# Kernel tuning notes

Hardware: AMD Instinct MI355X
Metric: run time of the kernel (lower is better)

The kernel has to match this reference:

```python
import jax, jax.numpy as jnp
import numpy as np

HEADS = 16
DIM_HEAD = 64
SCALE = DIM_HEAD ** -0.5


def setup_inputs() -> dict:
    key = jax.random.key(0)
    ks = jax.random.split(key, 7)
    b, n, m, d = 2, 2048, 2048, 1024
    inner = HEADS * DIM_HEAD  # 1024
    patch_embed = jax.random.normal(ks[0], (b, n, d), dtype=jnp.float32)
    pixel_embed = jax.random.normal(ks[1], (b, m, d), dtype=jnp.float32)
    s = 1.0 / np.sqrt(d)
    Wq = jax.random.normal(ks[2], (d, inner), dtype=jnp.float32) * s
    Wk = jax.random.normal(ks[3], (d, inner), dtype=jnp.float32) * s
    Wv = jax.random.normal(ks[4], (d, inner), dtype=jnp.float32) * s
    Wo = jax.random.normal(ks[5], (inner, d), dtype=jnp.float32) * (1.0 / np.sqrt(inner))
    bo = jax.random.normal(ks[6], (d,), dtype=jnp.float32) * 0.01
    return {"patch_embed": patch_embed, "pixel_embed": pixel_embed,
            "Wq": Wq, "Wk": Wk, "Wv": Wv, "Wo": Wo, "bo": bo}


def reference(patch_embed, pixel_embed, Wq, Wk, Wv, Wo, bo):
    b, n, _ = patch_embed.shape
    h, dh = HEADS, DIM_HEAD
    # projections
    q = patch_embed @ Wq  # [b, n, h*dh]
    k = pixel_embed @ Wk  # [b, m, h*dh]
    v = pixel_embed @ Wv  # [b, m, h*dh]
    # split heads: [b, seq, h, dh]
    q = q.reshape(b, n, h, dh)
    k = k.reshape(b, -1, h, dh)
    v = v.reshape(b, -1, h, dh)
    sim = jnp.einsum('bihd,bjhd->bhij', q, k) * SCALE  # [b, h, n, m]
    attn = jax.nn.softmax(sim, axis=-1)
    out = jnp.einsum('bhij,bjhd->bihd', attn, v)  # [b, n, h, dh]
    out = out.reshape(b, n, h * dh)
    return out @ Wo + bo  # [b, n, query_dim]
```

## Files before the change

kernel.cpp:

```cpp
#include <hip/hip_runtime.h>

#define SEQ 2048
#define DMODEL 1024
#define HEADS 16
#define DH 64
#define QSCALE 0.180336880f

typedef __attribute__((ext_vector_type(8))) short short8;
typedef __attribute__((ext_vector_type(4))) float f32x4;
typedef __attribute__((ext_vector_type(16))) float f32x16;
typedef __attribute__((ext_vector_type(2))) unsigned int uint2v;
typedef __attribute__((ext_vector_type(4))) unsigned int uint4v;

__device__ __forceinline__ ushort f2bf(float x) {
  union { float f; unsigned u; } v; v.f = x;
  return (ushort)((v.u + 0x7fffu + ((v.u >> 16) & 1u)) >> 16);
}

__device__ __forceinline__ void gld16(const ushort* g, ushort* l) {
  __builtin_amdgcn_global_load_lds(
      (const __attribute__((address_space(1))) unsigned int*)g,
      (__attribute__((address_space(3))) unsigned int*)l, 16, 0, 0);
}

__global__ __launch_bounds__(256) void prologue(
    const float* __restrict__ patch, const float* __restrict__ pixel,
    const float* __restrict__ W0, const float* __restrict__ W1,
    const float* __restrict__ W2, const float* __restrict__ W3,
    ushort* __restrict__ pb, ushort* __restrict__ xb,
    ushort* __restrict__ O0, ushort* __restrict__ O1,
    ushort* __restrict__ O2, ushort* __restrict__ O3) {
  const int z = blockIdx.z;
  const int tx = threadIdx.x, ty = threadIdx.y;
  if (z < 2) {
    const float4* in = (const float4*)(z ? pixel : patch);
    ushort4* out = (ushort4*)(z ? xb : pb);
    const int base = (blockIdx.y * 32 + blockIdx.x) * 256 + ty * 32 + tx;
#pragma unroll
    for (int rep = 0; rep < 4; ++rep) {
      const int i = base + rep * 262144;
      float4 f = in[i];
      out[i] = make_ushort4(f2bf(f.x), f2bf(f.y), f2bf(f.z), f2bf(f.w));
    }
    return;
  }
  __shared__ float tile[32][33];
  const int zz = z - 2;
  const float* in = zz == 0 ? W0 : zz == 1 ? W1 : zz == 2 ? W2 : W3;
  ushort* out = zz == 0 ? O0 : zz == 1 ? O1 : zz == 2 ? O2 : O3;
  const float scale = zz == 0 ? QSCALE : 1.0f;
  const int n0 = blockIdx.x * 32, k0 = blockIdx.y * 32;
#pragma unroll
  for (int i = 0; i < 4; ++i)
    tile[ty + i * 8][tx] = in[(size_t)(k0 + ty + i * 8) * DMODEL + n0 + tx];
  __syncthreads();
#pragma unroll
  for (int i = 0; i < 4; ++i)
    out[(size_t)(n0 + ty + i * 8) * DMODEL + k0 + tx] =
        f2bf(tile[tx][ty + i * 8] * scale);
}

__global__ __launch_bounds__(256) void mfma_gemm_qkv(
    const ushort* __restrict__ pb, const ushort* __restrict__ xb,
    const ushort* __restrict__ wqt, const ushort* __restrict__ wkt,
    const ushort* __restrict__ wvt, ushort* __restrict__ qws,
    ushort* __restrict__ kws, ushort* __restrict__ vws) {
  __shared__ __align__(16) ushort As[128 * 64];
  __shared__ __align__(16) ushort Bs[128 * 64];
  const int z = blockIdx.z;
  const ushort* A = (z == 0) ? pb : xb;
  const ushort* Bt = (z == 0) ? wqt : (z == 1) ? wkt : wvt;

  const int t = threadIdx.x;
  const int w = t >> 6, lane = t & 63, ln = lane & 15, q = lane >> 4;
  const int wm = w & 1, wn = w >> 1;
  const int row0 = blockIdx.y * 128, col0 = blockIdx.x * 128;
  const int sw = ln & 7;

  f32x4 acc[4][4];
#pragma unroll
  for (int i = 0; i < 4; ++i)
#pragma unroll
    for (int j = 0; j < 4; ++j) acc[i][j] = (f32x4){0.f, 0.f, 0.f, 0.f};

  for (int k0 = 0; k0 < DMODEL; k0 += 64) {
    __syncthreads();
#pragma unroll
    for (int rep = 0; rep < 4; ++rep) {
      const int u0 = rep * 256 + w * 64;
      const int u = u0 + lane;
      const int r = u >> 3, gl = (u & 7) ^ (r & 7);
      gld16(&A[(size_t)(row0 + r) * DMODEL + k0 + gl * 8], &As[u0 * 8]);
      gld16(&Bt[(size_t)(col0 + r) * DMODEL + k0 + gl * 8], &Bs[u0 * 8]);
    }
    __syncthreads();
#pragma unroll
    for (int ks = 0; ks < 2; ++ks) {
      short8 af[4], bf[4];
#pragma unroll
      for (int rt = 0; rt < 4; ++rt)
        af[rt] = *(const short8*)&As[(wm * 64 + rt * 16 + ln) * 64 +
                                     (((ks * 4 + q) ^ sw) * 8)];
#pragma unroll
      for (int ct = 0; ct < 4; ++ct)
        bf[ct] = *(const short8*)&Bs[(wn * 64 + ct * 16 + ln) * 64 +
                                     (((ks * 4 + q) ^ sw) * 8)];
#pragma unroll
      for (int rt = 0; rt < 4; ++rt)
#pragma unroll
        for (int ct = 0; ct < 4; ++ct)
          acc[rt][ct] = __builtin_amdgcn_mfma_f32_16x16x32_bf16(af[rt], bf[ct],
                                                                acc[rt][ct], 0, 0, 0);
    }
  }

  if (z < 2) {
    ushort* dst = z == 0 ? qws : kws;
#pragma unroll
    for (int rt = 0; rt < 4; ++rt)
#pragma unroll
      for (int ct = 0; ct < 4; ++ct) {
        const int c = col0 + wn * 64 + ct * 16 + ln;
#pragma unroll
        for (int reg = 0; reg < 4; ++reg) {
          const int r = row0 + wm * 64 + rt * 16 + q * 4 + reg;
          dst[(size_t)r * DMODEL + c] = f2bf(acc[rt][ct][reg]);
        }
      }
  } else {
#pragma unroll
    for (int rt = 0; rt < 4; ++rt)
#pragma unroll
      for (int ct = 0; ct < 4; ++ct) {
        const int c = col0 + wn * 64 + ct * 16 + ln;
        const int hh = c >> 6, d = c & 63;
        const int r0 = row0 + wm * 64 + rt * 16 + q * 4;
        const int bb = r0 >> 11, s0 = r0 & (SEQ - 1);
        ushort4 u4 = make_ushort4(f2bf(acc[rt][ct][0]), f2bf(acc[rt][ct][1]),
                                  f2bf(acc[rt][ct][2]), f2bf(acc[rt][ct][3]));
        *(ushort4*)&vws[((size_t)(bb * HEADS + hh) * DH + d) * SEQ + s0] = u4;
      }
  }
}

__global__ __launch_bounds__(256, 2) void flash_mfma(
    const ushort* __restrict__ Qg, const ushort* __restrict__ Kg,
    const ushort* __restrict__ Vg, ushort* __restrict__ Og) {
  __shared__ __align__(16) ushort Kst[2][64 * 64];
  __shared__ __align__(16) ushort Vst[2][64 * 64];

  const int t = threadIdx.x;
  const int w = t >> 6, lane = t & 63;
  const int l31 = lane & 31, hi = lane >> 5, l7 = lane & 7, l8 = lane >> 3;
  const int bh = blockIdx.x;
  const int qt = blockIdx.y;
  const int b = bh >> 4, h = bh & 15;

  const ushort* qrow = Qg + ((size_t)b * SEQ) * DMODEL + h * DH;
  const ushort* krow = Kg + ((size_t)b * SEQ) * DMODEL + h * DH;
  const ushort* vg = Vg + (size_t)bh * DH * SEQ;

  short8 qf[4];
#pragma unroll
  for (int ks = 0; ks < 4; ++ks)
    qf[ks] = *(const short8*)
        &qrow[(size_t)(qt * 128 + w * 32 + l31) * DMODEL + ks * 16 + hi * 8];

  f32x16 acc_o[2];
#pragma unroll
  for (int db = 0; db < 2; ++db)
#pragma unroll
    for (int e = 0; e < 16; ++e) acc_o[db][e] = 0.f;
  float l_i = 0.f;

  const int fbase = (w & 1) * 4;
  const bool isV = (w >= 2);
  const int swz = (l7 ^ l8) * 8;

  {
#pragma unroll
    for (int i = 0; i < 4; ++i) {
      const int f = fbase + i;
      if (!isV)
        gld16(&krow[(size_t)(f * 8 + l8) * DMODEL + swz], &Kst[0][f * 512]);
      else
        gld16(&vg[(size_t)(f * 8 + l8) * SEQ + swz], &Vst[0][f * 512]);
    }
  }
  __syncthreads();

  for (int kt = 0; kt < SEQ / 64; ++kt) {
    const int cur = kt & 1;
    if (kt + 1 < SEQ / 64) {
#pragma unroll
      for (int i = 0; i < 4; ++i) {
        const int f = fbase + i;
        if (!isV)
          gld16(&krow[(size_t)((kt + 1) * 64 + f * 8 + l8) * DMODEL + swz],
                &Kst[cur ^ 1][f * 512]);
        else
          gld16(&vg[(size_t)(f * 8 + l8) * SEQ + (kt + 1) * 64 + swz],
                &Vst[cur ^ 1][f * 512]);
      }
    }

    const ushort* Kc = &Kst[cur][0];
    const ushort* Vc = &Vst[cur][0];

    f32x16 accs[2];
#pragma unroll
    for (int kb = 0; kb < 2; ++kb)
#pragma unroll
      for (int e = 0; e < 16; ++e) accs[kb][e] = 0.f;
#pragma unroll
    for (int kb = 0; kb < 2; ++kb)
#pragma unroll
      for (int ks = 0; ks < 4; ++ks) {
        const short8 kf = *(const short8*)
            &Kc[(kb * 32 + l31) * 64 + (((ks * 2 + hi) ^ l7) * 8)];
        accs[kb] = __builtin_amdgcn_mfma_f32_32x32x16_bf16(kf, qf[ks],
                                                           accs[kb], 0, 0, 0);
      }

    short8 vf[4][2];
#pragma unroll
    for (int sg = 0; sg < 4; ++sg)
#pragma unroll
      for (int db = 0; db < 2; ++db)
        vf[sg][db] = *(const short8*)
            &Vc[(db * 32 + l31) * 64 + (((sg * 2 + hi) ^ l7) * 8)];

#pragma unroll
    for (int kb = 0; kb < 2; ++kb)
#pragma unroll
      for (int e = 0; e < 16; ++e) {
        const float p = __builtin_amdgcn_exp2f(accs[kb][e]);
        accs[kb][e] = p;
        l_i += p;
      }

    short8 pa[4];
#pragma unroll
    for (int kb = 0; kb < 2; ++kb) {
      unsigned wq[4][2];
#pragma unroll
      for (int o = 0; o < 4; ++o) {
        asm("v_cvt_pk_bf16_f32 %0, %1, %2"
            : "=v"(wq[o][0])
            : "v"(accs[kb][4 * o + 0]), "v"(accs[kb][4 * o + 1]));
        asm("v_cvt_pk_bf16_f32 %0, %1, %2"
            : "=v"(wq[o][1])
            : "v"(accs[kb][4 * o + 2]), "v"(accs[kb][4 * o + 3]));
      }
#pragma unroll
      for (int sl = 0; sl < 2; ++sl) {
        uint2v r02 = __builtin_amdgcn_permlane32_swap(wq[2 * sl][0],
                                                      wq[2 * sl + 1][0],
                                                      false, false);
        uint2v r13 = __builtin_amdgcn_permlane32_swap(wq[2 * sl][1],
                                                      wq[2 * sl + 1][1],
                                                      false, false);
        uint4v pk = {r02.x, r13.x, r02.y, r13.y};
        pa[kb * 2 + sl] = __builtin_bit_cast(short8, pk);
      }
    }

#pragma unroll
    for (int sg = 0; sg < 4; ++sg)
#pragma unroll
      for (int db = 0; db < 2; ++db)
        acc_o[db] = __builtin_amdgcn_mfma_f32_32x32x16_bf16(pa[sg], vf[sg][db],
                                                            acc_o[db], 0, 0, 0);

    __syncthreads();
  }

  l_i += __shfl_xor(l_i, 32);
  const float inv = 1.0f / l_i;
#pragma unroll
  for (int o = 0; o < 4; ++o)
#pragma unroll
    for (int r0 = 0; r0 < 4; ++r0) {
      const int row = o * 8 + r0 + 4 * hi;
      const float invr = __shfl(inv, row, 64);
      const int s = qt * 128 + w * 32 + row;
#pragma unroll
      for (int db = 0; db < 2; ++db)
        Og[(size_t)(b * SEQ + s) * DMODEL + h * DH + db * 32 + l31] =
            f2bf(acc_o[db][4 * o + r0] * invr);
    }
}

__global__ __launch_bounds__(256) void mfma_gemm_out(const ushort* __restrict__ A,
                                                     const ushort* __restrict__ Bt,
                                                     const float* __restrict__ bias,
                                                     float* __restrict__ dst) {
  __shared__ __align__(16) ushort As[64 * 64];
  __shared__ __align__(16) ushort Bs[128 * 64];
  const int t = threadIdx.x;
  const int w = t >> 6, lane = t & 63, ln = lane & 15, q = lane >> 4;
  const int wm = w & 1, wn = w >> 1;
  const int row0 = blockIdx.y * 64, col0 = blockIdx.x * 128;
  const int sw = ln & 7;

  f32x4 acc[2][4];
#pragma unroll
  for (int i = 0; i < 2; ++i)
#pragma unroll
    for (int j = 0; j < 4; ++j) acc[i][j] = (f32x4){0.f, 0.f, 0.f, 0.f};

  for (int k0 = 0; k0 < DMODEL; k0 += 64) {
    __syncthreads();
#pragma unroll
    for (int rep = 0; rep < 2; ++rep) {
      const int u0 = rep * 256 + w * 64;
      const int u = u0 + lane;
      const int r = u >> 3, gl = (u & 7) ^ (r & 7);
      gld16(&A[(size_t)(row0 + r) * DMODEL + k0 + gl * 8], &As[u0 * 8]);
    }
#pragma unroll
    for (int rep = 0; rep < 4; ++rep) {
      const int u0 = rep * 256 + w * 64;
      const int u = u0 + lane;
      const int r = u >> 3, gl = (u & 7) ^ (r & 7);
      gld16(&Bt[(size_t)(col0 + r) * DMODEL + k0 + gl * 8], &Bs[u0 * 8]);
    }
    __syncthreads();
#pragma unroll
    for (int ks = 0; ks < 2; ++ks) {
      short8 af[2], bf[4];
#pragma unroll
      for (int rt = 0; rt < 2; ++rt)
        af[rt] = *(const short8*)&As[(wm * 32 + rt * 16 + ln) * 64 +
                                     (((ks * 4 + q) ^ sw) * 8)];
#pragma unroll
      for (int ct = 0; ct < 4; ++ct)
        bf[ct] = *(const short8*)&Bs[(wn * 64 + ct * 16 + ln) * 64 +
                                     (((ks * 4 + q) ^ sw) * 8)];
#pragma unroll
      for (int rt = 0; rt < 2; ++rt)
#pragma unroll
        for (int ct = 0; ct < 4; ++ct)
          acc[rt][ct] = __builtin_amdgcn_mfma_f32_16x16x32_bf16(af[rt], bf[ct],
                                                                acc[rt][ct], 0, 0, 0);
    }
  }

#pragma unroll
  for (int rt = 0; rt < 2; ++rt)
#pragma unroll
    for (int ct = 0; ct < 4; ++ct) {
      const int c = col0 + wn * 64 + ct * 16 + ln;
      const float bi = bias[c];
#pragma unroll
      for (int reg = 0; reg < 4; ++reg) {
        const int r = row0 + wm * 32 + rt * 16 + q * 4 + reg;
        dst[(size_t)r * DMODEL + c] = acc[rt][ct][reg] + bi;
      }
    }
}

extern "C" void kernel_launch(void* const* d_in, const int* in_sizes, int n_in,
                              void* d_out, int out_size, void* d_ws,
                              size_t ws_size, hipStream_t stream) {
  const float* patch = (const float*)d_in[0];
  const float* pixel = (const float*)d_in[1];
  const float* Wq = (const float*)d_in[2];
  const float* Wk = (const float*)d_in[3];
  const float* Wv = (const float*)d_in[4];
  const float* Wo = (const float*)d_in[5];
  const float* bo = (const float*)d_in[6];
  float* out = (float*)d_out;

  const size_t E = (size_t)2 * SEQ * DMODEL;
  const size_t W = (size_t)DMODEL * DMODEL;
  ushort* pb  = (ushort*)d_ws;
  ushort* xb  = pb + E;
  ushort* wqt = xb + E;
  ushort* wkt = wqt + W;
  ushort* wvt = wkt + W;
  ushort* wot = wvt + W;
  ushort* qws = wot + W;
  ushort* kws = qws + E;
  ushort* vws = kws + E;
  ushort* aws = vws + E;

  prologue<<<dim3(32, 32, 6), dim3(32, 8), 0, stream>>>(
      patch, pixel, Wq, Wk, Wv, Wo, pb, xb, wqt, wkt, wvt, wot);
  mfma_gemm_qkv<<<dim3(8, 32, 3), 256, 0, stream>>>(pb, xb, wqt, wkt, wvt,
                                                    qws, kws, vws);
  flash_mfma<<<dim3(32, 16), 256, 0, stream>>>(qws, kws, vws, aws);
  mfma_gemm_out<<<dim3(8, 64), 256, 0, stream>>>(aws, wot, bo, out);
}
```

Before: 190.8 us.

## Deepen flash attention K/V staging to four-buffer pipeline with vmcnt waits

Replaces the double-buffered K/V shared-memory staging with a four-slot ring that prefetches three tiles ahead. The loop is unrolled by four, and the full __syncthreads is replaced with explicit s_waitcnt vmcnt plus s_barrier so only the oldest tile's loads must land before compute. The change also adds s_setprio around the MFMA blocks and starts the first QK MFMA from a zero vector instead of zeroing accumulators. Shared memory doubles to 64KB per block, which may limit the two-blocks-per-CU occupancy target.

```diff
diff --git a/kernel.cpp b/kernel.cpp
--- a/kernel.cpp
+++ b/kernel.cpp
@@ -146,8 +146,8 @@
 __global__ __launch_bounds__(256, 2) void flash_mfma(
     const ushort* __restrict__ Qg, const ushort* __restrict__ Kg,
     const ushort* __restrict__ Vg, ushort* __restrict__ Og) {
-  __shared__ __align__(16) ushort Kst[2][64 * 64];
-  __shared__ __align__(16) ushort Vst[2][64 * 64];
+  __shared__ __align__(16) ushort Kst[4][64 * 64];
+  __shared__ __align__(16) ushort Vst[4][64 * 64];
 
   const int t = threadIdx.x;
   const int w = t >> 6, lane = t & 63;
@@ -173,107 +173,113 @@
     for (int e = 0; e < 16; ++e) acc_o[db][e] = 0.f;
   float l_i = 0.f;
 
+  f32x16 ZERO;
+#pragma unroll
+  for (int e = 0; e < 16; ++e) ZERO[e] = 0.f;
+
   const int fbase = (w & 1) * 4;
   const bool isV = (w >= 2);
   const int swz = (l7 ^ l8) * 8;
 
-  {
-#pragma unroll
-    for (int i = 0; i < 4; ++i) {
-      const int f = fbase + i;
-      if (!isV)
-        gld16(&krow[(size_t)(f * 8 + l8) * DMODEL + swz], &Kst[0][f * 512]);
-      else
-        gld16(&vg[(size_t)(f * 8 + l8) * SEQ + swz], &Vst[0][f * 512]);
-    }
-  }
-  __syncthreads();
-
-  for (int kt = 0; kt < SEQ / 64; ++kt) {
-    const int cur = kt & 1;
-    if (kt + 1 < SEQ / 64) {
+  auto stage = [&](int tile, ushort* Kb, ushort* Vb) {
+    if (!isV) {
 #pragma unroll
       for (int i = 0; i < 4; ++i) {
         const int f = fbase + i;
-        if (!isV)
-          gld16(&krow[(size_t)((kt + 1) * 64 + f * 8 + l8) * DMODEL + swz],
-                &Kst[cur ^ 1][f * 512]);
-        else
-          gld16(&vg[(size_t)(f * 8 + l8) * SEQ + (kt + 1) * 64 + swz],
-                &Vst[cur ^ 1][f * 512]);
+        gld16(&krow[(size_t)(tile * 64 + f * 8 + l8) * DMODEL + swz],
+              &Kb[f * 512]);
       }
-    }
-
-    const ushort* Kc = &Kst[cur][0];
-    const ushort* Vc = &Vst[cur][0];
-
-    f32x16 accs[2];
-#pragma unroll
-    for (int kb = 0; kb < 2; ++kb)
-#pragma unroll
-      for (int e = 0; e < 16; ++e) accs[kb][e] = 0.f;
-#pragma unroll
-    for (int kb = 0; kb < 2; ++kb)
-#pragma unroll
-      for (int ks = 0; ks < 4; ++ks) {
-        const short8 kf = *(const short8*)
-            &Kc[(kb * 32 + l31) * 64 + (((ks * 2 + hi) ^ l7) * 8)];
-        accs[kb] = __builtin_amdgcn_mfma_f32_32x32x16_bf16(kf, qf[ks],
-                                                           accs[kb], 0, 0, 0);
+    } else {
+#pragma unroll
+      for (int i = 0; i < 4; ++i) {
+        const int f = fbase + i;
+        gld16(&vg[(size_t)(f * 8 + l8) * SEQ + tile * 64 + swz],
+              &Vb[f * 512]);
       }
-
-    short8 vf[4][2];
-#pragma unroll
-    for (int sg = 0; sg < 4; ++sg)
-#pragma unroll
-      for (int db = 0; db < 2; ++db)
-        vf[sg][db] = *(const short8*)
-            &Vc[(db * 32 + l31) * 64 + (((sg * 2 + hi) ^ l7) * 8)];
-
-#pragma unroll
-    for (int kb = 0; kb < 2; ++kb)
-#pragma unroll
-      for (int e = 0; e < 16; ++e) {
-        const float p = __builtin_amdgcn_exp2f(accs[kb][e]);
-        accs[kb][e] = p;
-        l_i += p;
-      }
-
-    short8 pa[4];
-#pragma unroll
-    for (int kb = 0; kb < 2; ++kb) {
-      unsigned wq[4][2];
-#pragma unroll
-      for (int o = 0; o < 4; ++o) {
-        asm("v_cvt_pk_bf16_f32 %0, %1, %2"
-            : "=v"(wq[o][0])
-            : "v"(accs[kb][4 * o + 0]), "v"(accs[kb][4 * o + 1]));
-        asm("v_cvt_pk_bf16_f32 %0, %1, %2"
-            : "=v"(wq[o][1])
-            : "v"(accs[kb][4 * o + 2]), "v"(accs[kb][4 * o + 3]));
-      }
-#pragma unroll
-      for (int sl = 0; sl < 2; ++sl) {
-        uint2v r02 = __builtin_amdgcn_permlane32_swap(wq[2 * sl][0],
-                                                      wq[2 * sl + 1][0],
-                                                      false, false);
-        uint2v r13 = __builtin_amdgcn_permlane32_swap(wq[2 * sl][1],
-                                                      wq[2 * sl + 1][1],
-                                                      false, false);
-        uint4v pk = {r02.x, r13.x, r02.y, r13.y};
-        pa[kb * 2 + sl] = __builtin_bit_cast(short8, pk);
-      }
-    }
-
-#pragma unroll
-    for (int sg = 0; sg < 4; ++sg)
-#pragma unroll
-      for (int db = 0; db < 2; ++db)
-        acc_o[db] = __builtin_amdgcn_mfma_f32_32x32x16_bf16(pa[sg], vf[sg][db],
-                                                            acc_o[db], 0, 0, 0);
-
-    __syncthreads();
-  }
+    }
+  };
+
+  stage(0, Kst[0], Vst[0]);
+  stage(1, Kst[1], Vst[1]);
+  stage(2, Kst[2], Vst[2]);
+  asm volatile("s_waitcnt vmcnt(8)" ::: "memory");
+  __builtin_amdgcn_s_barrier();
+  __builtin_amdgcn_sched_barrier(0);
+
+#define FLASH_STEP(BUF, PFTILE, DOPF, VMN, DOBAR)                            \
+  {                                                                          \
+    if (DOPF) stage((PFTILE), Kst[((BUF) + 3) & 3], Vst[((BUF) + 3) & 3]);   \
+    const ushort* Kc = Kst[(BUF)];                                           \
+    const ushort* Vc = Vst[(BUF)];                                           \
+    f32x16 accs[2];                                                          \
+    __builtin_amdgcn_s_setprio(1);                                           \
+    _Pragma("unroll") for (int kb = 0; kb < 2; ++kb) {                       \
+      accs[kb] = __builtin_amdgcn_mfma_f32_32x32x16_bf16(                    \
+          *(const short8*)&Kc[(kb * 32 + l31) * 64 + ((hi ^ l7) * 8)],       \
+          qf[0], ZERO, 0, 0, 0);                                             \
+      _Pragma("unroll") for (int ks = 1; ks < 4; ++ks) {                     \
+        const short8 kf = *(const short8*)                                   \
+            &Kc[(kb * 32 + l31) * 64 + (((ks * 2 + hi) ^ l7) * 8)];          \
+        accs[kb] = __builtin_amdgcn_mfma_f32_32x32x16_bf16(                  \
+            kf, qf[ks], accs[kb], 0, 0, 0);                                  \
+      }                                                                      \
+    }                                                                        \
+    __builtin_amdgcn_s_setprio(0);                                           \
+    short8 vf[4][2];                                                         \
+    _Pragma("unroll") for (int sg = 0; sg < 4; ++sg)                         \
+      _Pragma("unroll") for (int db = 0; db < 2; ++db)                       \
+        vf[sg][db] = *(const short8*)                                        \
+            &Vc[(db * 32 + l31) * 64 + (((sg * 2 + hi) ^ l7) * 8)];          \
+    _Pragma("unroll") for (int kb = 0; kb < 2; ++kb)                         \
+      _Pragma("unroll") for (int e = 0; e < 16; ++e) {                       \
+        const float p = __builtin_amdgcn_exp2f(accs[kb][e]);                 \
+        accs[kb][e] = p;                                                     \
+        l_i += p;                                                            \
+      }                                                                      \
+    short8 pa[4];                                                            \
+    _Pragma("unroll") for (int kb = 0; kb < 2; ++kb) {                       \
+      unsigned wq[4][2];                                                     \
+      _Pragma("unroll") for (int o = 0; o < 4; ++o) {                        \
+        asm("v_cvt_pk_bf16_f32 %0, %1, %2"                                   \
+            : "=v"(wq[o][0])                                                 \
+            : "v"(accs[kb][4 * o + 0]), "v"(accs[kb][4 * o + 1]));           \
+        asm("v_cvt_pk_bf16_f32 %0, %1, %2"                                   \
+            : "=v"(wq[o][1])                                                 \
+            : "v"(accs[kb][4 * o + 2]), "v"(accs[kb][4 * o + 3]));           \
+      }                                                                      \
+      _Pragma("unroll") for (int sl = 0; sl < 2; ++sl) {                     \
+        uint2v r02 = __builtin_amdgcn_permlane32_swap(                       \
+            wq[2 * sl][0], wq[2 * sl + 1][0], false, false);                 \
+        uint2v r13 = __builtin_amdgcn_permlane32_swap(                       \
+            wq[2 * sl][1], wq[2 * sl + 1][1], false, false);                 \
+        uint4v pk = {r02.x, r13.x, r02.y, r13.y};                            \
+        pa[kb * 2 + sl] = __builtin_bit_cast(short8, pk);                    \
+      }                                                                      \
+    }                                                                        \
+    __builtin_amdgcn_s_setprio(1);                                           \
+    _Pragma("unroll") for (int sg = 0; sg < 4; ++sg)                         \
+      _Pragma("unroll") for (int db = 0; db < 2; ++db)                       \
+        acc_o[db] = __builtin_amdgcn_mfma_f32_32x32x16_bf16(                 \
+            pa[sg], vf[sg][db], acc_o[db], 0, 0, 0);                         \
+    __builtin_amdgcn_s_setprio(0);                                           \
+    if (DOBAR) {                                                             \
+      asm volatile("s_waitcnt vmcnt(" #VMN ")" ::: "memory");                \
+      __builtin_amdgcn_s_barrier();                                          \
+      __builtin_amdgcn_sched_barrier(0);                                     \
+    }                                                                        \
+  }
+
+  for (int kt = 0; kt < 28; kt += 4) {
+    FLASH_STEP(0, kt + 3, true, 8, true);
+    FLASH_STEP(1, kt + 4, true, 8, true);
+    FLASH_STEP(2, kt + 5, true, 8, true);
+    FLASH_STEP(3, kt + 6, true, 8, true);
+  }
+  FLASH_STEP(0, 31, true, 8, true);
+  FLASH_STEP(1, 0, false, 4, true);
+  FLASH_STEP(2, 0, false, 0, true);
+  FLASH_STEP(3, 0, false, 0, false);
+#undef FLASH_STEP
 
   l_i += __shfl_xor(l_i, 32);
   const float inv = 1.0f / l_i;
```

Measured after the change: 199.3 us. 4.4% more time.

## Split flash attention waves across query and key halves with LDS reduction

Applied to the files above, without the earlier changes.

Each wave now handles 64 query rows and half of each 64-key tile, instead of 32 query rows and the full tile. K fragments are reused across two query blocks and each wave reads only half the V fragments, which cuts LDS read traffic per MFMA. Partial outputs and row sums from the two key halves are combined through a new 32KB+ shared-memory reduction at the end. The extra LDS footprint (about 33KB) may lower occupancy under launch_bounds(256,2), and the larger accumulators raise register pressure.

```diff
diff --git a/kernel.cpp b/kernel.cpp
--- a/kernel.cpp
+++ b/kernel.cpp
@@ -148,10 +148,13 @@
     const ushort* __restrict__ Vg, ushort* __restrict__ Og) {
   __shared__ __align__(16) ushort Kst[2][64 * 64];
   __shared__ __align__(16) ushort Vst[2][64 * 64];
+  __shared__ float Red[2][4096];
+  __shared__ float Redl[2][64];
 
   const int t = threadIdx.x;
   const int w = t >> 6, lane = t & 63;
   const int l31 = lane & 31, hi = lane >> 5, l7 = lane & 7, l8 = lane >> 3;
+  const int qh = w & 1, kh = w >> 1;
   const int bh = blockIdx.x;
   const int qt = blockIdx.y;
   const int b = bh >> 4, h = bh & 15;
@@ -160,32 +163,35 @@
   const ushort* krow = Kg + ((size_t)b * SEQ) * DMODEL + h * DH;
   const ushort* vg = Vg + (size_t)bh * DH * SEQ;
 
-  short8 qf[4];
-#pragma unroll
-  for (int ks = 0; ks < 4; ++ks)
-    qf[ks] = *(const short8*)
-        &qrow[(size_t)(qt * 128 + w * 32 + l31) * DMODEL + ks * 16 + hi * 8];
-
-  f32x16 acc_o[2];
-#pragma unroll
-  for (int db = 0; db < 2; ++db)
-#pragma unroll
-    for (int e = 0; e < 16; ++e) acc_o[db][e] = 0.f;
-  float l_i = 0.f;
+  short8 qf[2][4];
+#pragma unroll
+  for (int qb = 0; qb < 2; ++qb)
+#pragma unroll
+    for (int ks = 0; ks < 4; ++ks)
+      qf[qb][ks] = *(const short8*)
+          &qrow[(size_t)(qt * 128 + qh * 64 + qb * 32 + l31) * DMODEL +
+                ks * 16 + hi * 8];
+
+  f32x16 acc_o[2][2];
+#pragma unroll
+  for (int qb = 0; qb < 2; ++qb)
+#pragma unroll
+    for (int db = 0; db < 2; ++db)
+#pragma unroll
+      for (int e = 0; e < 16; ++e) acc_o[qb][db][e] = 0.f;
+  float l_i[2] = {0.f, 0.f};
 
   const int fbase = (w & 1) * 4;
   const bool isV = (w >= 2);
   const int swz = (l7 ^ l8) * 8;
 
-  {
-#pragma unroll
-    for (int i = 0; i < 4; ++i) {
-      const int f = fbase + i;
-      if (!isV)
-        gld16(&krow[(size_t)(f * 8 + l8) * DMODEL + swz], &Kst[0][f * 512]);
-      else
-        gld16(&vg[(size_t)(f * 8 + l8) * SEQ + swz], &Vst[0][f * 512]);
-    }
+#pragma unroll
+  for (int i = 0; i < 4; ++i) {
+    const int f = fbase + i;
+    if (!isV)
+      gld16(&krow[(size_t)(f * 8 + l8) * DMODEL + swz], &Kst[0][f * 512]);
+    else
+      gld16(&vg[(size_t)(f * 8 + l8) * SEQ + swz], &Vst[0][f * 512]);
   }
   __syncthreads();
 
@@ -209,48 +215,48 @@
 
     f32x16 accs[2];
 #pragma unroll
-    for (int kb = 0; kb < 2; ++kb)
-#pragma unroll
-      for (int e = 0; e < 16; ++e) accs[kb][e] = 0.f;
-#pragma unroll
-    for (int kb = 0; kb < 2; ++kb)
-#pragma unroll
-      for (int ks = 0; ks < 4; ++ks) {
-        const short8 kf = *(const short8*)
-            &Kc[(kb * 32 + l31) * 64 + (((ks * 2 + hi) ^ l7) * 8)];
-        accs[kb] = __builtin_amdgcn_mfma_f32_32x32x16_bf16(kf, qf[ks],
-                                                           accs[kb], 0, 0, 0);
-      }
-
-    short8 vf[4][2];
-#pragma unroll
-    for (int sg = 0; sg < 4; ++sg)
+    for (int qb = 0; qb < 2; ++qb)
+#pragma unroll
+      for (int e = 0; e < 16; ++e) accs[qb][e] = 0.f;
+#pragma unroll
+    for (int ks = 0; ks < 4; ++ks) {
+      const short8 kf = *(const short8*)
+          &Kc[(kh * 32 + l31) * 64 + (((ks * 2 + hi) ^ l7) * 8)];
+#pragma unroll
+      for (int qb = 0; qb < 2; ++qb)
+        accs[qb] = __builtin_amdgcn_mfma_f32_32x32x16_bf16(kf, qf[qb][ks],
+                                                           accs[qb], 0, 0, 0);
+    }
+
+    short8 vf[2][2];
+#pragma unroll
+    for (int sl = 0; sl < 2; ++sl)
 #pragma unroll
       for (int db = 0; db < 2; ++db)
-        vf[sg][db] = *(const short8*)
-            &Vc[(db * 32 + l31) * 64 + (((sg * 2 + hi) ^ l7) * 8)];
-
-#pragma unroll
-    for (int kb = 0; kb < 2; ++kb)
+        vf[sl][db] = *(const short8*)
+            &Vc[(db * 32 + l31) * 64 + (((kh * 4 + sl * 2 + hi) ^ l7) * 8)];
+
+#pragma unroll
+    for (int qb = 0; qb < 2; ++qb)
 #pragma unroll
       for (int e = 0; e < 16; ++e) {
-        const float p = __builtin_amdgcn_exp2f(accs[kb][e]);
-        accs[kb][e] = p;
-        l_i += p;
-      }
-
-    short8 pa[4];
-#pragma unroll
-    for (int kb = 0; kb < 2; ++kb) {
+        const float p = __builtin_amdgcn_exp2f(accs[qb][e]);
+        accs[qb][e] = p;
+        l_i[qb] += p;
+      }
+
+    short8 pa[2][2];
+#pragma unroll
+    for (int qb = 0; qb < 2; ++qb) {
       unsigned wq[4][2];
 #pragma unroll
       for (int o = 0; o < 4; ++o) {
         asm("v_cvt_pk_bf16_f32 %0, %1, %2"
             : "=v"(wq[o][0])
-            : "v"(accs[kb][4 * o + 0]), "v"(accs[kb][4 * o + 1]));
+            : "v"(accs[qb][4 * o + 0]), "v"(accs[qb][4 * o + 1]));
         asm("v_cvt_pk_bf16_f32 %0, %1, %2"
             : "=v"(wq[o][1])
-            : "v"(accs[kb][4 * o + 2]), "v"(accs[kb][4 * o + 3]));
+            : "v"(accs[qb][4 * o + 2]), "v"(accs[qb][4 * o + 3]));
       }
 #pragma unroll
       for (int sl = 0; sl < 2; ++sl) {
@@ -261,34 +267,66 @@
                                                       wq[2 * sl + 1][1],
                                                       false, false);
         uint4v pk = {r02.x, r13.x, r02.y, r13.y};
-        pa[kb * 2 + sl] = __builtin_bit_cast(short8, pk);
-      }
-    }
-
-#pragma unroll
-    for (int sg = 0; sg < 4; ++sg)
+        pa[qb][sl] = __builtin_bit_cast(short8, pk);
+      }
+    }
+
+#pragma unroll
+    for (int sl = 0; sl < 2; ++sl)
 #pragma unroll
       for (int db = 0; db < 2; ++db)
-        acc_o[db] = __builtin_amdgcn_mfma_f32_32x32x16_bf16(pa[sg], vf[sg][db],
-                                                            acc_o[db], 0, 0, 0);
+#pragma unroll
+        for (int qb = 0; qb < 2; ++qb)
+          acc_o[qb][db] = __builtin_amdgcn_mfma_f32_32x32x16_bf16(
+              pa[qb][sl], vf[sl][db], acc_o[qb][db], 0, 0, 0);
 
     __syncthreads();
   }
 
-  l_i += __shfl_xor(l_i, 32);
-  const float inv = 1.0f / l_i;
-#pragma unroll
-  for (int o = 0; o < 4; ++o)
-#pragma unroll
-    for (int r0 = 0; r0 < 4; ++r0) {
-      const int row = o * 8 + r0 + 4 * hi;
-      const float invr = __shfl(inv, row, 64);
-      const int s = qt * 128 + w * 32 + row;
+  l_i[0] += __shfl_xor(l_i[0], 32);
+  l_i[1] += __shfl_xor(l_i[1], 32);
+
+  if (kh == 1) {
+#pragma unroll
+    for (int qb = 0; qb < 2; ++qb) {
 #pragma unroll
       for (int db = 0; db < 2; ++db)
-        Og[(size_t)(b * SEQ + s) * DMODEL + h * DH + db * 32 + l31] =
-            f2bf(acc_o[db][4 * o + r0] * invr);
-    }
+#pragma unroll
+        for (int e = 0; e < 16; ++e)
+          Red[qh][((qb * 2 + db) * 32 + hi * 16 + e) * 32 + l31] =
+              acc_o[qb][db][e];
+      if (hi == 0) Redl[qh][qb * 32 + l31] = l_i[qb];
+    }
+  }
+  __syncthreads();
+  if (kh == 0) {
+    float inv[2];
+#pragma unroll
+    for (int qb = 0; qb < 2; ++qb)
+      inv[qb] = 1.0f / (l_i[qb] + Redl[qh][qb * 32 + l31]);
+#pragma unroll
+    for (int qb = 0; qb < 2; ++qb)
+#pragma unroll
+      for (int db = 0; db < 2; ++db)
+#pragma unroll
+        for (int e = 0; e < 16; ++e)
+          acc_o[qb][db][e] +=
+              Red[qh][((qb * 2 + db) * 32 + hi * 16 + e) * 32 + l31];
+#pragma unroll
+    for (int qb = 0; qb < 2; ++qb)
+#pragma unroll
+      for (int o = 0; o < 4; ++o)
+#pragma unroll
+        for (int r0 = 0; r0 < 4; ++r0) {
+          const int row = o * 8 + r0 + 4 * hi;
+          const float invr = __shfl(inv[qb], row, 64);
+          const int s = qt * 128 + qh * 64 + qb * 32 + row;
+#pragma unroll
+          for (int db = 0; db < 2; ++db)
+            Og[(size_t)(b * SEQ + s) * DMODEL + h * DH + db * 32 + l31] =
+                f2bf(acc_o[qb][db][4 * o + r0] * invr);
+        }
+  }
 }
 
 __global__ __launch_bounds__(256) void mfma_gemm_out(const ushort* __restrict__ A,
```

After: 196.3 us. 2.9% more time.

## Process two KV tiles per iteration in flash attention to overlap softmax with MFMA

Applied to the files above, without the earlier changes.

The flash attention loop now stages and processes pairs of 64-row K/V tiles per iteration, which halves the number of barriers. It interleaves the QK MFMAs of both tiles and schedules tile A's PV MFMAs before tile B's exp/pack, so matrix and VALU work can overlap. The row-sum accumulator is split into four partial sums to shorten the dependency chain. In exchange, shared memory doubles to 64KB per block and register pressure rises, which may hurt occupancy at the 2-blocks-per-SM launch bound.

```diff
diff --git a/kernel.cpp b/kernel.cpp
--- a/kernel.cpp
+++ b/kernel.cpp
@@ -146,8 +146,8 @@
 __global__ __launch_bounds__(256, 2) void flash_mfma(
     const ushort* __restrict__ Qg, const ushort* __restrict__ Kg,
     const ushort* __restrict__ Vg, ushort* __restrict__ Og) {
-  __shared__ __align__(16) ushort Kst[2][64 * 64];
-  __shared__ __align__(16) ushort Vst[2][64 * 64];
+  __shared__ __align__(16) ushort Kst[2][2][64 * 64];
+  __shared__ __align__(16) ushort Vst[2][2][64 * 64];
 
   const int t = threadIdx.x;
   const int w = t >> 6, lane = t & 63;
@@ -171,110 +171,132 @@
   for (int db = 0; db < 2; ++db)
 #pragma unroll
     for (int e = 0; e < 16; ++e) acc_o[db][e] = 0.f;
-  float l_i = 0.f;
+  float l4[4] = {0.f, 0.f, 0.f, 0.f};
 
   const int fbase = (w & 1) * 4;
   const bool isV = (w >= 2);
   const int swz = (l7 ^ l8) * 8;
 
-  {
-#pragma unroll
-    for (int i = 0; i < 4; ++i) {
-      const int f = fbase + i;
-      if (!isV)
-        gld16(&krow[(size_t)(f * 8 + l8) * DMODEL + swz], &Kst[0][f * 512]);
-      else
-        gld16(&vg[(size_t)(f * 8 + l8) * SEQ + swz], &Vst[0][f * 512]);
-    }
-  }
-  __syncthreads();
-
-  for (int kt = 0; kt < SEQ / 64; ++kt) {
-    const int cur = kt & 1;
-    if (kt + 1 < SEQ / 64) {
+  auto stagePair = [&](int pt, int buf) {
+#pragma unroll
+    for (int st2 = 0; st2 < 2; ++st2) {
+      const int tile = pt * 2 + st2;
 #pragma unroll
       for (int i = 0; i < 4; ++i) {
         const int f = fbase + i;
         if (!isV)
-          gld16(&krow[(size_t)((kt + 1) * 64 + f * 8 + l8) * DMODEL + swz],
-                &Kst[cur ^ 1][f * 512]);
+          gld16(&krow[(size_t)(tile * 64 + f * 8 + l8) * DMODEL + swz],
+                &Kst[buf][st2][f * 512]);
         else
-          gld16(&vg[(size_t)(f * 8 + l8) * SEQ + (kt + 1) * 64 + swz],
-                &Vst[cur ^ 1][f * 512]);
-      }
-    }
-
-    const ushort* Kc = &Kst[cur][0];
-    const ushort* Vc = &Vst[cur][0];
-
-    f32x16 accs[2];
+          gld16(&vg[(size_t)(f * 8 + l8) * SEQ + tile * 64 + swz],
+                &Vst[buf][st2][f * 512]);
+      }
+    }
+  };
+
+  stagePair(0, 0);
+  __syncthreads();
+
+  for (int pt = 0; pt < SEQ / 128; ++pt) {
+    const int cur = pt & 1;
+    if (pt + 1 < SEQ / 128) stagePair(pt + 1, cur ^ 1);
+
+    const ushort* KcA = &Kst[cur][0][0];
+    const ushort* KcB = &Kst[cur][1][0];
+    const ushort* VcA = &Vst[cur][0][0];
+    const ushort* VcB = &Vst[cur][1][0];
+
+    f32x16 accsA[2], accsB[2];
 #pragma unroll
     for (int kb = 0; kb < 2; ++kb)
 #pragma unroll
-      for (int e = 0; e < 16; ++e) accs[kb][e] = 0.f;
+      for (int e = 0; e < 16; ++e) {
+        accsA[kb][e] = 0.f;
+        accsB[kb][e] = 0.f;
+      }
 #pragma unroll
     for (int kb = 0; kb < 2; ++kb)
 #pragma unroll
       for (int ks = 0; ks < 4; ++ks) {
-        const short8 kf = *(const short8*)
-            &Kc[(kb * 32 + l31) * 64 + (((ks * 2 + hi) ^ l7) * 8)];
-        accs[kb] = __builtin_amdgcn_mfma_f32_32x32x16_bf16(kf, qf[ks],
-                                                           accs[kb], 0, 0, 0);
-      }
-
-    short8 vf[4][2];
+        const int off = (kb * 32 + l31) * 64 + (((ks * 2 + hi) ^ l7) * 8);
+        const short8 kfA = *(const short8*)&KcA[off];
+        accsA[kb] = __builtin_amdgcn_mfma_f32_32x32x16_bf16(kfA, qf[ks],
+                                                            accsA[kb], 0, 0, 0);
+        const short8 kfB = *(const short8*)&KcB[off];
+        accsB[kb] = __builtin_amdgcn_mfma_f32_32x32x16_bf16(kfB, qf[ks],
+                                                            accsB[kb], 0, 0, 0);
+      }
+
+    short8 vfA[4][2];
 #pragma unroll
     for (int sg = 0; sg < 4; ++sg)
 #pragma unroll
       for (int db = 0; db < 2; ++db)
-        vf[sg][db] = *(const short8*)
-            &Vc[(db * 32 + l31) * 64 + (((sg * 2 + hi) ^ l7) * 8)];
-
-#pragma unroll
-    for (int kb = 0; kb < 2; ++kb)
-#pragma unroll
-      for (int e = 0; e < 16; ++e) {
-        const float p = __builtin_amdgcn_exp2f(accs[kb][e]);
-        accs[kb][e] = p;
-        l_i += p;
-      }
-
-    short8 pa[4];
-#pragma unroll
-    for (int kb = 0; kb < 2; ++kb) {
-      unsigned wq[4][2];
-#pragma unroll
-      for (int o = 0; o < 4; ++o) {
-        asm("v_cvt_pk_bf16_f32 %0, %1, %2"
-            : "=v"(wq[o][0])
-            : "v"(accs[kb][4 * o + 0]), "v"(accs[kb][4 * o + 1]));
-        asm("v_cvt_pk_bf16_f32 %0, %1, %2"
-            : "=v"(wq[o][1])
-            : "v"(accs[kb][4 * o + 2]), "v"(accs[kb][4 * o + 3]));
-      }
-#pragma unroll
-      for (int sl = 0; sl < 2; ++sl) {
-        uint2v r02 = __builtin_amdgcn_permlane32_swap(wq[2 * sl][0],
-                                                      wq[2 * sl + 1][0],
-                                                      false, false);
-        uint2v r13 = __builtin_amdgcn_permlane32_swap(wq[2 * sl][1],
-                                                      wq[2 * sl + 1][1],
-                                                      false, false);
-        uint4v pk = {r02.x, r13.x, r02.y, r13.y};
-        pa[kb * 2 + sl] = __builtin_bit_cast(short8, pk);
-      }
-    }
-
+        vfA[sg][db] = *(const short8*)
+            &VcA[(db * 32 + l31) * 64 + (((sg * 2 + hi) ^ l7) * 8)];
+
+#define SOFTMAX_PACK(ACCS, PA)                                               \
+  {                                                                          \
+    _Pragma("unroll") for (int kb = 0; kb < 2; ++kb)                         \
+        _Pragma("unroll") for (int e = 0; e < 16; ++e) {                     \
+      const float p = __builtin_amdgcn_exp2f(ACCS[kb][e]);                   \
+      ACCS[kb][e] = p;                                                       \
+      l4[e & 3] += p;                                                        \
+    }                                                                        \
+    _Pragma("unroll") for (int kb = 0; kb < 2; ++kb) {                       \
+      unsigned wq[4][2];                                                     \
+      _Pragma("unroll") for (int o = 0; o < 4; ++o) {                        \
+        asm("v_cvt_pk_bf16_f32 %0, %1, %2"                                   \
+            : "=v"(wq[o][0])                                                 \
+            : "v"(ACCS[kb][4 * o + 0]), "v"(ACCS[kb][4 * o + 1]));           \
+        asm("v_cvt_pk_bf16_f32 %0, %1, %2"                                   \
+            : "=v"(wq[o][1])                                                 \
+            : "v"(ACCS[kb][4 * o + 2]), "v"(ACCS[kb][4 * o + 3]));           \
+      }                                                                      \
+      _Pragma("unroll") for (int sl = 0; sl < 2; ++sl) {                     \
+        uint2v r02 = __builtin_amdgcn_permlane32_swap(                       \
+            wq[2 * sl][0], wq[2 * sl + 1][0], false, false);                 \
+        uint2v r13 = __builtin_amdgcn_permlane32_swap(                       \
+            wq[2 * sl][1], wq[2 * sl + 1][1], false, false);                 \
+        uint4v pk = {r02.x, r13.x, r02.y, r13.y};                            \
+        PA[kb * 2 + sl] = __builtin_bit_cast(short8, pk);                    \
+      }                                                                      \
+    }                                                                        \
+  }
+
+    short8 paA[4];
+    SOFTMAX_PACK(accsA, paA);
+
+    short8 vfB[4][2];
 #pragma unroll
     for (int sg = 0; sg < 4; ++sg)
 #pragma unroll
       for (int db = 0; db < 2; ++db)
-        acc_o[db] = __builtin_amdgcn_mfma_f32_32x32x16_bf16(pa[sg], vf[sg][db],
-                                                            acc_o[db], 0, 0, 0);
+        vfB[sg][db] = *(const short8*)
+            &VcB[(db * 32 + l31) * 64 + (((sg * 2 + hi) ^ l7) * 8)];
+
+#pragma unroll
+    for (int sg = 0; sg < 4; ++sg)
+#pragma unroll
+      for (int db = 0; db < 2; ++db)
+        acc_o[db] = __builtin_amdgcn_mfma_f32_32x32x16_bf16(
+            paA[sg], vfA[sg][db], acc_o[db], 0, 0, 0);
+
+    short8 paB[4];
+    SOFTMAX_PACK(accsB, paB);
+#undef SOFTMAX_PACK
+
+#pragma unroll
+    for (int sg = 0; sg < 4; ++sg)
+#pragma unroll
+      for (int db = 0; db < 2; ++db)
+        acc_o[db] = __builtin_amdgcn_mfma_f32_32x32x16_bf16(
+            paB[sg], vfB[sg][db], acc_o[db], 0, 0, 0);
 
     __syncthreads();
   }
 
+  float l_i = (l4[0] + l4[1]) + (l4[2] + l4[3]);
   l_i += __shfl_xor(l_i, 32);
   const float inv = 1.0f / l_i;
 #pragma unroll
```

Result: no change. 190.5 us (-0.2%).
